# Kernel optimization log

Measured on AMD Instinct MI355X. Metric: run time of the kernel, lower is better.

Reference implementation:

```python
import jax, jax.numpy as jnp
import numpy as np

CHUNK = 128  # chunk size for the chunked causal linear-attention scan
EPS = 1e-6


def _feature_map(x):
    # elu(x) + 1, matching torch.nn.functional.elu (alpha=1)
    return jax.nn.elu(x) + 1.0


def _causal_linear(Q, K, V):
    """Chunked causal linear attention.

    Q, K: [N, H, L, D], V: [N, H, L, Dv] (float32).
    Computes out[l] = Q[l] @ sum_{s<=l} K[s]^T V[s] without materializing
    the O(L*D*Dv) cumulative outer-product tensor.
    """
    N, H, L, D = Q.shape
    Dv = V.shape[-1]
    C = L // CHUNK
    # [C, N, H, T, D]
    qc = jnp.moveaxis(Q.reshape(N, H, C, CHUNK, D), 2, 0)
    kc = jnp.moveaxis(K.reshape(N, H, C, CHUNK, D), 2, 0)
    vc = jnp.moveaxis(V.reshape(N, H, C, CHUNK, Dv), 2, 0)
    tri = jnp.tril(jnp.ones((CHUNK, CHUNK), dtype=Q.dtype))  # causal mask within chunk

    def step(S, qkv):
        q, k, v = qkv  # [N, H, T, D], [N, H, T, D], [N, H, T, Dv]
        attn = jnp.einsum('nhtd,nhsd->nhts', q, k) * tri
        out = jnp.einsum('nhts,nhse->nhte', attn, v) \
            + jnp.einsum('nhtd,nhde->nhte', q, S)
        S = S + jnp.einsum('nhsd,nhse->nhde', k, v)
        return S, out

    S0 = jnp.zeros((N, H, D, Dv), dtype=Q.dtype)
    _, outs = jax.lax.scan(step, S0, (qc, kc, vc))  # outs: [C, N, H, T, Dv]
    return jnp.moveaxis(outs, 0, 2).reshape(N, H, L, Dv)


def setup_inputs() -> dict:
    key = jax.random.key(0)
    kq, kk, kv = jax.random.split(key, 3)
    shape = (4, 8192, 8, 64)  # [N, L, H, D]
    return {
        'queries': jax.random.normal(kq, shape, dtype=jnp.float32),
        'keys': jax.random.normal(kk, shape, dtype=jnp.float32),
        'values': jax.random.normal(kv, shape, dtype=jnp.float32),
    }


def reference(queries, keys, values):
    dtype = queries.dtype
    Q = _feature_map(queries)  # [N, L, H, D]
    K = _feature_map(keys)
    # normalizer: Z = 1 / (Q . cumsum_l(K) + eps), shape [N, L, H]
    Z = 1.0 / (jnp.einsum('nlhi,nlhi->nlh', Q, jnp.cumsum(K, axis=1)) + EPS)
    # numerator computed in float32 per original causal_linear
    Qf = jnp.transpose(Q, (0, 2, 1, 3)).astype(jnp.float32)
    Kf = jnp.transpose(K, (0, 2, 1, 3)).astype(jnp.float32)
    Vf = jnp.transpose(values, (0, 2, 1, 3)).astype(jnp.float32)
    Vn = _causal_linear(Qf, Kf, Vf)  # [N, H, L, Dv]
    Vn = jnp.transpose(Vn, (0, 2, 1, 3)).astype(dtype)  # [N, L, H, Dv]
    return Vn * Z[:, :, :, None]
```

## Files before the change

### kernel.cpp

```cpp
#include <hip/hip_runtime.h>
#include <math.h>

#define N_    4
#define L_    8192
#define H_    8
#define NH_   32
#define CHK   64
#define NC_   128
#define ROWF  512
#define EPSF  1e-6f

typedef __attribute__((ext_vector_type(8))) short bf16x8;
typedef __attribute__((ext_vector_type(4))) float f32x4;
typedef __attribute__((ext_vector_type(4))) unsigned short us4;

__device__ __forceinline__ float fmap(float x) { return x > 0.f ? x + 1.f : __expf(x); }

__device__ __forceinline__ unsigned short f2bf(float x) {
  unsigned u = __float_as_uint(x);
  u += 0x7FFFu + ((u >> 16) & 1u);
  return (unsigned short)(u >> 16);
}
__device__ __forceinline__ float bf2f(unsigned short u) {
  return __uint_as_float(((unsigned)u) << 16);
}

__device__ __forceinline__ int sidx(int row, int col) {
  return row * 64 + (col ^ ((row & 7) << 3));
}

__device__ __forceinline__ f32x4 MFMA(bf16x8 a, bf16x8 b, f32x4 c) {
  return __builtin_amdgcn_mfma_f32_16x16x32_bf16(a, b, c, 0, 0, 0);
}

__global__ __launch_bounds__(256) void k_chunk_tot(const float* __restrict__ keys,
                                                   const float* __restrict__ values,
                                                   unsigned short* __restrict__ Tws,
                                                   float* __restrict__ Kcs) {
  __shared__ unsigned short Kt[64 * 64];
  __shared__ unsigned short Vt[64 * 64];
  __shared__ float kacc[64];
  const int bid = blockIdx.x;
  const int nh = bid / NC_, c = bid % NC_;
  const int n = nh / H_, h = nh % H_;
  const int tid = threadIdx.x;
  const int lane = tid & 63;
  const int wv = tid >> 6;
  const int lane15 = lane & 15, lg = lane >> 4;
  const int arow = wv * 16 + lane15;

  if (tid < 64) kacc[tid] = 0.f;

  float kpart = 0.f;
  {
    const int d = tid & 63, sg = tid >> 6;
    const size_t gbase = ((size_t)(n * L_ + c * CHK)) * ROWF + h * 64 + d;
    for (int rep = 0; rep < 4; ++rep) {
      const int s0 = (sg * 4 + rep) * 4;
      us4 wk, wvv;
#pragma unroll
      for (int j = 0; j < 4; ++j) {
        const size_t g = gbase + (size_t)(s0 + j) * ROWF;
        const float kf = fmap(keys[g]);
        kpart += kf;
        wk[j] = f2bf(kf);
        wvv[j] = f2bf(values[g]);
      }
      *(us4*)&Kt[sidx(d, s0)] = wk;
      *(us4*)&Vt[sidx(d, s0)] = wvv;
    }
  }
  __syncthreads();

  atomicAdd(&kacc[tid & 63], kpart);

  const bf16x8 av0 = *(const bf16x8*)&Vt[sidx(arow, lg * 8)];
  const bf16x8 av1 = *(const bf16x8*)&Vt[sidx(arow, (lg + 4) * 8)];
  unsigned short* Tp = Tws + (size_t)bid * 4096;
#pragma unroll
  for (int nt = 0; nt < 4; ++nt) {
    const int brow = nt * 16 + lane15;
    f32x4 acc = {0.f, 0.f, 0.f, 0.f};
    acc = MFMA(*(const bf16x8*)&Kt[sidx(brow, lg * 8)], av0, acc);
    acc = MFMA(*(const bf16x8*)&Kt[sidx(brow, (lg + 4) * 8)], av1, acc);
    us4 w;
#pragma unroll
    for (int r = 0; r < 4; ++r) w[r] = f2bf(acc[r]);
    *(us4*)&Tp[(size_t)arow * 64 + nt * 16 + lg * 4] = w;
  }
  __syncthreads();
  if (tid < 64) Kcs[(size_t)bid * 64 + tid] = kacc[tid];
}

__global__ __launch_bounds__(256) void k_scan(unsigned short* __restrict__ Tws,
                                              float* __restrict__ Kcs) {
  const int tid = threadIdx.x;
  if (blockIdx.x < 512) {
    const int gid = blockIdx.x * 256 + tid;
    const int nh = gid >> 12, de = gid & 4095;
    unsigned short* p = Tws + (size_t)nh * NC_ * 4096 + de;
    float run = 0.f;
    for (int s = 0; s < 32; ++s) {
      const float x0 = bf2f(p[(size_t)(s * 4 + 0) * 4096]);
      const float x1 = bf2f(p[(size_t)(s * 4 + 1) * 4096]);
      const float x2 = bf2f(p[(size_t)(s * 4 + 2) * 4096]);
      const float x3 = bf2f(p[(size_t)(s * 4 + 3) * 4096]);
      p[(size_t)(s * 4 + 0) * 4096] = f2bf(run);
      p[(size_t)(s * 4 + 1) * 4096] = f2bf(run + x0);
      p[(size_t)(s * 4 + 2) * 4096] = f2bf(run + x0 + x1);
      p[(size_t)(s * 4 + 3) * 4096] = f2bf(run + x0 + x1 + x2);
      run += x0 + x1 + x2 + x3;
    }
  } else {
    const int gid = (blockIdx.x - 512) * 256 + tid;
    const int nh = gid >> 6, d = gid & 63;
    float* p = Kcs + (size_t)nh * NC_ * 64 + d;
    float run = 0.f;
    for (int s = 0; s < 32; ++s) {
      const float x0 = p[(size_t)(s * 4 + 0) * 64];
      const float x1 = p[(size_t)(s * 4 + 1) * 64];
      const float x2 = p[(size_t)(s * 4 + 2) * 64];
      const float x3 = p[(size_t)(s * 4 + 3) * 64];
      p[(size_t)(s * 4 + 0) * 64] = run;
      p[(size_t)(s * 4 + 1) * 64] = run + x0;
      p[(size_t)(s * 4 + 2) * 64] = run + x0 + x1;
      p[(size_t)(s * 4 + 3) * 64] = run + x0 + x1 + x2;
      run += x0 + x1 + x2 + x3;
    }
  }
}

__global__ __launch_bounds__(256, 6) void k_output(const float* __restrict__ queries,
                                                   const float* __restrict__ keys,
                                                   const float* __restrict__ values,
                                                   const unsigned short* __restrict__ Pws,
                                                   const float* __restrict__ Kpre,
                                                   float* __restrict__ out) {
  __shared__ unsigned short Ks[64 * 64];
  __shared__ unsigned short Vt[64 * 64];
  __shared__ unsigned short St[64 * 64];
  __shared__ float kpre[64];

  const int wg = blockIdx.x;
  const int bid = (wg & 7) * (NH_ * NC_ / 8) + (wg >> 3);
  const int nh = bid / NC_, c = bid % NC_;
  const int n = nh / H_, h = nh % H_;
  const int tid = threadIdx.x;
  const int lane = tid & 63;
  const int wv = tid >> 6;
  const int lane15 = lane & 15, lg = lane >> 4;
  const int t0w = wv * 16;
  const int trow = t0w + lane15;
  const int l0 = c * CHK;

  {
    const int r0 = tid >> 4, c4 = (tid & 15) * 4;
    for (int rep = 0; rep < 4; ++rep) {
      const int row = r0 + rep * 16;
      const size_t g = ((size_t)(n * L_ + l0 + row)) * ROWF + h * 64 + c4;
      const float4 k = *(const float4*)&keys[g];
      us4 uk;
      uk[0] = f2bf(fmap(k.x)); uk[1] = f2bf(fmap(k.y));
      uk[2] = f2bf(fmap(k.z)); uk[3] = f2bf(fmap(k.w));
      *(us4*)&Ks[sidx(row, c4)] = uk;
    }
  }
  {
    const int d = tid & 63, sg = tid >> 6;
    const size_t gbase = ((size_t)(n * L_ + l0)) * ROWF + h * 64 + d;
    for (int rep = 0; rep < 4; ++rep) {
      const int s0 = (sg * 4 + rep) * 4;
      us4 w;
#pragma unroll
      for (int j = 0; j < 4; ++j) w[j] = f2bf(values[gbase + (size_t)(s0 + j) * ROWF]);
      *(us4*)&Vt[sidx(d, s0)] = w;
    }
  }
  {
    const unsigned short* pp = Pws + (size_t)bid * 4096;
    const int r0 = tid >> 4, c4 = (tid & 15) * 4;
    for (int rep = 0; rep < 4; ++rep) {
      const int row = r0 + rep * 16;
      *(us4*)&St[sidx(row, c4)] = *(const us4*)&pp[row * 64 + c4];
    }
  }
  if (tid < 64) kpre[tid] = Kpre[(size_t)bid * 64 + tid];
  bf16x8 qf0, qf1;
  {
    const size_t qg = ((size_t)(n * L_ + l0 + trow)) * ROWF + h * 64;
    const float4 a = *(const float4*)&queries[qg + lg * 8];
    const float4 b = *(const float4*)&queries[qg + lg * 8 + 4];
    const float4 cc = *(const float4*)&queries[qg + 32 + lg * 8];
    const float4 d4 = *(const float4*)&queries[qg + 32 + lg * 8 + 4];
    qf0[0] = (short)f2bf(fmap(a.x)); qf0[1] = (short)f2bf(fmap(a.y));
    qf0[2] = (short)f2bf(fmap(a.z)); qf0[3] = (short)f2bf(fmap(a.w));
    qf0[4] = (short)f2bf(fmap(b.x)); qf0[5] = (short)f2bf(fmap(b.y));
    qf0[6] = (short)f2bf(fmap(b.z)); qf0[7] = (short)f2bf(fmap(b.w));
    qf1[0] = (short)f2bf(fmap(cc.x)); qf1[1] = (short)f2bf(fmap(cc.y));
    qf1[2] = (short)f2bf(fmap(cc.z)); qf1[3] = (short)f2bf(fmap(cc.w));
    qf1[4] = (short)f2bf(fmap(d4.x)); qf1[5] = (short)f2bf(fmap(d4.y));
    qf1[6] = (short)f2bf(fmap(d4.z)); qf1[7] = (short)f2bf(fmap(d4.w));
  }
  __syncthreads();

  f32x4 aT[4];
#pragma unroll
  for (int nt = 0; nt < 4; ++nt) {
    const int srow = nt * 16 + lane15;
    f32x4 a = {0.f, 0.f, 0.f, 0.f};
    a = MFMA(*(const bf16x8*)&Ks[sidx(srow, lg * 8)], qf0, a);
    a = MFMA(*(const bf16x8*)&Ks[sidx(srow, (lg + 4) * 8)], qf1, a);
    aT[nt] = a;
  }
  float zp = 0.f;
#pragma unroll
  for (int j = 0; j < 8; ++j) zp += bf2f((unsigned short)qf0[j]) * kpre[lg * 8 + j];
#pragma unroll
  for (int j = 0; j < 8; ++j) zp += bf2f((unsigned short)qf1[j]) * kpre[32 + lg * 8 + j];

  __syncthreads();

  float rs = 0.f;
#pragma unroll
  for (int nt = 0; nt < 4; ++nt) {
    us4 w;
#pragma unroll
    for (int r = 0; r < 4; ++r) {
      const int s = nt * 16 + lg * 4 + r;
      const float v = (s <= trow) ? aT[nt][r] : 0.f;
      rs += v;
      w[r] = f2bf(v);
    }
    *(us4*)&Ks[sidx(trow, nt * 16 + lg * 4)] = w;
  }
  float den = rs + zp;
  den += __shfl_xor(den, 16);
  den += __shfl_xor(den, 32);
  const float zv = 1.f / (den + EPSF);

  const bf16x8 af0 = *(const bf16x8*)&Ks[sidx(trow, lg * 8)];
  const bf16x8 af1 = *(const bf16x8*)&Ks[sidx(trow, 32 + lg * 8)];
  const size_t obase = ((size_t)(n * L_ + l0 + trow)) * ROWF + h * 64;
#pragma unroll
  for (int nt = 0; nt < 4; ++nt) {
    const int brow = nt * 16 + lane15;
    f32x4 o = {0.f, 0.f, 0.f, 0.f};
    o = MFMA(*(const bf16x8*)&Vt[sidx(brow, lg * 8)], af0, o);
    o = MFMA(*(const bf16x8*)&Vt[sidx(brow, (lg + 4) * 8)], af1, o);
    o = MFMA(*(const bf16x8*)&St[sidx(brow, lg * 8)], qf0, o);
    o = MFMA(*(const bf16x8*)&St[sidx(brow, (lg + 4) * 8)], qf1, o);
    const float4 w = make_float4(o[0] * zv, o[1] * zv, o[2] * zv, o[3] * zv);
    *(float4*)&out[obase + nt * 16 + lg * 4] = w;
  }
}

extern "C" void kernel_launch(void* const* d_in, const int* in_sizes, int n_in,
                              void* d_out, int out_size, void* d_ws, size_t ws_size,
                              hipStream_t stream) {
  const float* queries = (const float*)d_in[0];
  const float* keys    = (const float*)d_in[1];
  const float* values  = (const float*)d_in[2];
  float* out = (float*)d_out;

  const size_t t_elems = (size_t)NH_ * NC_ * 4096;
  const size_t k_elems = (size_t)NH_ * NC_ * 64;
  if (ws_size < t_elems * 2 + k_elems * 4) return;
  unsigned short* Tws = (unsigned short*)d_ws;
  float* Kcs = (float*)(Tws + t_elems);

  hipLaunchKernelGGL(k_chunk_tot, dim3(NH_ * NC_), dim3(256), 0, stream, keys, values, Tws, Kcs);
  hipLaunchKernelGGL(k_scan, dim3(512 + 8), dim3(256), 0, stream, Tws, Kcs);
  hipLaunchKernelGGL(k_output, dim3(NH_ * NC_), dim3(256), 0, stream,
                     queries, keys, values, Tws, Kcs, out);
}
```

Measured before the change: 96.21 us.

## Stage feature-mapped bf16 K/V tiles in workspace for output kernel reuse

The chunk-totals kernel now also writes the bf16 feature-mapped K tile (transposed) and the bf16 V tile, both already swizzled, to workspace. The output kernel copies these tiles and the prefix-state tile straight into shared memory with 16-byte loads, instead of re-reading the fp32 keys and values and recomputing the feature map. This halves the bytes the output kernel reads for K/V and removes strided scalar gathers, at the cost of extra workspace writes in the first kernel and a larger workspace requirement.

```diff
diff --git a/kernel.cpp b/kernel.cpp
--- a/kernel.cpp
+++ b/kernel.cpp
@@ -36,9 +36,11 @@
 __global__ __launch_bounds__(256) void k_chunk_tot(const float* __restrict__ keys,
                                                    const float* __restrict__ values,
                                                    unsigned short* __restrict__ Tws,
+                                                   unsigned short* __restrict__ Khat,
+                                                   unsigned short* __restrict__ Vhat,
                                                    float* __restrict__ Kcs) {
-  __shared__ unsigned short Kt[64 * 64];
-  __shared__ unsigned short Vt[64 * 64];
+  __shared__ __align__(16) unsigned short Kt[64 * 64];
+  __shared__ __align__(16) unsigned short Vt[64 * 64];
   __shared__ float kacc[64];
   const int bid = blockIdx.x;
   const int nh = bid / NC_, c = bid % NC_;
@@ -55,6 +57,7 @@
   {
     const int d = tid & 63, sg = tid >> 6;
     const size_t gbase = ((size_t)(n * L_ + c * CHK)) * ROWF + h * 64 + d;
+    unsigned short* Vp = Vhat + (size_t)bid * 4096;
     for (int rep = 0; rep < 4; ++rep) {
       const int s0 = (sg * 4 + rep) * 4;
       us4 wk, wvv;
@@ -68,6 +71,7 @@
       }
       *(us4*)&Kt[sidx(d, s0)] = wk;
       *(us4*)&Vt[sidx(d, s0)] = wvv;
+      *(us4*)&Vp[sidx(d, s0)] = wvv;
     }
   }
   __syncthreads();
@@ -86,7 +90,22 @@
     us4 w;
 #pragma unroll
     for (int r = 0; r < 4; ++r) w[r] = f2bf(acc[r]);
-    *(us4*)&Tp[(size_t)arow * 64 + nt * 16 + lg * 4] = w;
+    *(us4*)&Tp[sidx(arow, nt * 16 + lg * 4)] = w;
+  }
+
+  {
+    unsigned short* Kp = Khat + (size_t)bid * 4096;
+    const int s = tid >> 2, dd4 = (tid & 3) * 16;
+    unsigned short val[16];
+#pragma unroll
+    for (int m = 0; m < 16; ++m) val[m] = Kt[sidx(dd4 + m, s)];
+#pragma unroll
+    for (int q = 0; q < 4; ++q) {
+      us4 w;
+#pragma unroll
+      for (int r = 0; r < 4; ++r) w[r] = val[q * 4 + r];
+      *(us4*)&Kp[sidx(s, dd4 + q * 4)] = w;
+    }
   }
   __syncthreads();
   if (tid < 64) Kcs[(size_t)bid * 64 + tid] = kacc[tid];
@@ -131,14 +150,14 @@
 }
 
 __global__ __launch_bounds__(256, 6) void k_output(const float* __restrict__ queries,
-                                                   const float* __restrict__ keys,
-                                                   const float* __restrict__ values,
+                                                   const unsigned short* __restrict__ Khat,
+                                                   const unsigned short* __restrict__ Vhat,
                                                    const unsigned short* __restrict__ Pws,
                                                    const float* __restrict__ Kpre,
                                                    float* __restrict__ out) {
-  __shared__ unsigned short Ks[64 * 64];
-  __shared__ unsigned short Vt[64 * 64];
-  __shared__ unsigned short St[64 * 64];
+  __shared__ __align__(16) unsigned short Ks[64 * 64];
+  __shared__ __align__(16) unsigned short Vt[64 * 64];
+  __shared__ __align__(16) unsigned short St[64 * 64];
   __shared__ float kpre[64];
 
   const int wg = blockIdx.x;
@@ -153,38 +172,6 @@
   const int trow = t0w + lane15;
   const int l0 = c * CHK;
 
-  {
-    const int r0 = tid >> 4, c4 = (tid & 15) * 4;
-    for (int rep = 0; rep < 4; ++rep) {
-      const int row = r0 + rep * 16;
-      const size_t g = ((size_t)(n * L_ + l0 + row)) * ROWF + h * 64 + c4;
-      const float4 k = *(const float4*)&keys[g];
-      us4 uk;
-      uk[0] = f2bf(fmap(k.x)); uk[1] = f2bf(fmap(k.y));
-      uk[2] = f2bf(fmap(k.z)); uk[3] = f2bf(fmap(k.w));
-      *(us4*)&Ks[sidx(row, c4)] = uk;
-    }
-  }
-  {
-    const int d = tid & 63, sg = tid >> 6;
-    const size_t gbase = ((size_t)(n * L_ + l0)) * ROWF + h * 64 + d;
-    for (int rep = 0; rep < 4; ++rep) {
-      const int s0 = (sg * 4 + rep) * 4;
-      us4 w;
-#pragma unroll
-      for (int j = 0; j < 4; ++j) w[j] = f2bf(values[gbase + (size_t)(s0 + j) * ROWF]);
-      *(us4*)&Vt[sidx(d, s0)] = w;
-    }
-  }
-  {
-    const unsigned short* pp = Pws + (size_t)bid * 4096;
-    const int r0 = tid >> 4, c4 = (tid & 15) * 4;
-    for (int rep = 0; rep < 4; ++rep) {
-      const int row = r0 + rep * 16;
-      *(us4*)&St[sidx(row, c4)] = *(const us4*)&pp[row * 64 + c4];
-    }
-  }
-  if (tid < 64) kpre[tid] = Kpre[(size_t)bid * 64 + tid];
   bf16x8 qf0, qf1;
   {
     const size_t qg = ((size_t)(n * L_ + l0 + trow)) * ROWF + h * 64;
@@ -201,6 +188,17 @@
     qf1[4] = (short)f2bf(fmap(d4.x)); qf1[5] = (short)f2bf(fmap(d4.y));
     qf1[6] = (short)f2bf(fmap(d4.z)); qf1[7] = (short)f2bf(fmap(d4.w));
   }
+  {
+    const size_t tb = (size_t)bid * 4096;
+#pragma unroll
+    for (int it = 0; it < 2; ++it) {
+      const int i8 = (tid + it * 256) * 8;
+      *(uint4*)&Ks[i8] = *(const uint4*)&Khat[tb + i8];
+      *(uint4*)&Vt[i8] = *(const uint4*)&Vhat[tb + i8];
+      *(uint4*)&St[i8] = *(const uint4*)&Pws[tb + i8];
+    }
+  }
+  if (tid < 64) kpre[tid] = Kpre[(size_t)bid * 64 + tid];
   __syncthreads();
 
   f32x4 aT[4];
@@ -264,12 +262,15 @@
 
   const size_t t_elems = (size_t)NH_ * NC_ * 4096;
   const size_t k_elems = (size_t)NH_ * NC_ * 64;
-  if (ws_size < t_elems * 2 + k_elems * 4) return;
-  unsigned short* Tws = (unsigned short*)d_ws;
-  float* Kcs = (float*)(Tws + t_elems);
-
-  hipLaunchKernelGGL(k_chunk_tot, dim3(NH_ * NC_), dim3(256), 0, stream, keys, values, Tws, Kcs);
+  if (ws_size < t_elems * 2 * 3 + k_elems * 4) return;
+  unsigned short* Tws  = (unsigned short*)d_ws;
+  unsigned short* Khat = Tws + t_elems;
+  unsigned short* Vhat = Khat + t_elems;
+  float* Kcs = (float*)(Vhat + t_elems);
+
+  hipLaunchKernelGGL(k_chunk_tot, dim3(NH_ * NC_), dim3(256), 0, stream,
+                     keys, values, Tws, Khat, Vhat, Kcs);
   hipLaunchKernelGGL(k_scan, dim3(512 + 8), dim3(256), 0, stream, Tws, Kcs);
   hipLaunchKernelGGL(k_output, dim3(NH_ * NC_), dim3(256), 0, stream,
-                     queries, keys, values, Tws, Kcs, out);
-}
+                     queries, Khat, Vhat, Tws, Kcs, out);
+}
```

Result: slower. 136.3 us (+41.7%).
